# Optimization experiments

Hardware: AMD Instinct MI355X
Metric: run time of the kernel (lower is better)

## Reference

```python
import jax, jax.numpy as jnp
import numpy as np

N, E = 100000, 1600000
X_DIM, H_DIM, G_DIM = 128, 64, 64
Y_REP = H_DIM + G_DIM
N_OUT = 2


def setup_inputs() -> dict:
    key = jax.random.key(0)
    ks = jax.random.split(key, 16)
    features = jax.random.normal(ks[0], (N, X_DIM), dtype=jnp.float32)
    treatments = (jax.random.uniform(ks[1], (N,)) < 0.5).astype(jnp.float32)
    edge_index = jax.random.randint(ks[2], (2, E), 0, N, dtype=jnp.int64)
    s = 1.0 / np.sqrt(X_DIM)
    W_phi = jax.random.uniform(ks[3], (X_DIM, H_DIM), minval=-s, maxval=s, dtype=jnp.float32)
    b_phi = jax.random.uniform(ks[4], (H_DIM,), minval=-s, maxval=s, dtype=jnp.float32)
    sg = 1.0 / np.sqrt(H_DIM)
    W_gnn = jax.random.uniform(ks[5], (H_DIM, G_DIM), minval=-sg, maxval=sg, dtype=jnp.float32)
    b_gnn = jax.random.uniform(ks[6], (G_DIM,), minval=-sg, maxval=sg, dtype=jnp.float32)
    sy = 1.0 / np.sqrt(Y_REP)
    W00 = jax.random.uniform(ks[7], (N_OUT, Y_REP, Y_REP), minval=-sy, maxval=sy, dtype=jnp.float32)
    b00 = jax.random.uniform(ks[8], (N_OUT, Y_REP), minval=-sy, maxval=sy, dtype=jnp.float32)
    W10 = jax.random.uniform(ks[9], (N_OUT, Y_REP, Y_REP), minval=-sy, maxval=sy, dtype=jnp.float32)
    b10 = jax.random.uniform(ks[10], (N_OUT, Y_REP), minval=-sy, maxval=sy, dtype=jnp.float32)
    W01 = jax.random.uniform(ks[11], (Y_REP, 1), minval=-sy, maxval=sy, dtype=jnp.float32)
    b01 = jax.random.uniform(ks[12], (1,), minval=-sy, maxval=sy, dtype=jnp.float32)
    W11 = jax.random.uniform(ks[13], (Y_REP, 1), minval=-sy, maxval=sy, dtype=jnp.float32)
    b11 = jax.random.uniform(ks[14], (1,), minval=-sy, maxval=sy, dtype=jnp.float32)
    return dict(features=features, treatments=treatments, edge_index=edge_index,
                W_phi=W_phi, b_phi=b_phi, W_gnn=W_gnn, b_gnn=b_gnn,
                W00=W00, b00=b00, W10=W10, b10=b10,
                W01=W01, b01=b01, W11=W11, b11=b11)


def gcn_conv(x, edge_index, W, b, n_nodes):
    # PyG GCNConv defaults: add self-loops, symmetric deg^-1/2 normalization, bias.
    h = x @ W  # [N, G]
    loop = jnp.arange(n_nodes, dtype=edge_index.dtype)
    src = jnp.concatenate([edge_index[0], loop])
    dst = jnp.concatenate([edge_index[1], loop])
    deg = jax.ops.segment_sum(jnp.ones_like(dst, dtype=h.dtype), dst, num_segments=n_nodes)
    dinv = jnp.where(deg > 0, jax.lax.rsqrt(deg), 0.0)
    norm = dinv[src] * dinv[dst]  # [E+N]
    msg = h[src] * norm[:, None]  # gather + scale
    return jax.ops.segment_sum(msg, dst, num_segments=n_nodes) + b


def reference(features, treatments, edge_index, W_phi, b_phi, W_gnn, b_gnn,
              W00, b00, W10, b10, W01, b01, W11, b11):
    phi_x = jax.nn.relu(features @ W_phi + b_phi)  # [N, H]
    phi_x_t = treatments[:, None] * phi_x
    rep_gnn = gcn_conv(phi_x_t, edge_index, W_gnn, b_gnn, features.shape[0])  # [N, G]
    # dropout is a no-op in eval mode
    rep_post = jnp.concatenate([phi_x, rep_gnn], axis=1)  # [N, H+G]
    # faithful to the original: each iteration recomputes from rep_post (only last layer matters)
    for i in range(N_OUT):
        y00 = jax.nn.relu(rep_post @ W00[i] + b00[i])
        y10 = jax.nn.relu(rep_post @ W10[i] + b10[i])
    y0_pred = (y00 @ W01 + b01).reshape(-1)
    y1_pred = (y10 @ W11 + b11).reshape(-1)
    return y1_pred, y0_pred, phi_x
```

## Files before the change

### kernel.cpp

```cpp
#include <hip/hip_runtime.h>
#include <stdint.h>

typedef unsigned short u16;
typedef unsigned int u32;
typedef unsigned long long u64;
typedef long long ll;

#define XD 128
#define HD 64
#define GD 64
#define YREP 128
#define CAP 40

typedef __attribute__((ext_vector_type(8))) short bf16x8;
typedef __attribute__((ext_vector_type(4))) float f32x4;

#define SWT_LD  136
#define SF_LD   136
#define SO_LD   72

__device__ __forceinline__ float b2f(u16 x) { return __uint_as_float(((u32)x) << 16); }
__device__ __forceinline__ u16 f2b(float f) {
    u32 u = __float_as_uint(f);
    return (u16)((u + 0x7fffu + ((u >> 16) & 1u)) >> 16);
}
__device__ __forceinline__ float ldf(const void* p, size_t i, int bf) {
    return bf ? b2f(((const u16*)p)[i]) : ((const float*)p)[i];
}
__device__ __forceinline__ void stf(void* p, size_t i, float v, int bf) {
    if (bf) ((u16*)p)[i] = f2b(v);
    else ((float*)p)[i] = v;
}
__device__ __forceinline__ int ldi(const void* p, size_t i, int w) {
    return w ? (int)((const ll*)p)[i] : ((const int*)p)[i];
}
__device__ __forceinline__ bf16x8 ld_a8(const void* p, size_t off, int bf) {
    if (bf) return *(const bf16x8*)((const u16*)p + off);
    const float* fp = (const float*)p + off;
    bf16x8 a;
    #pragma unroll
    for (int i = 0; i < 8; ++i) a[i] = (short)f2b(fp[i]);
    return a;
}

__global__ void detect_kernel(const u32* __restrict__ treat_w,
                              const u32* __restrict__ eidx_w,
                              int* __restrict__ flags)
{
    int t = threadIdx.x;
    bool isbf = false, nzhi = false;
    for (int i = t; i < 256; i += 64) {
        isbf |= (treat_w[i] == 0x3F803F80u);
        nzhi |= (eidx_w[2 * i + 1] != 0u);
    }
    u64 mb = __ballot(isbf);
    u64 mn = __ballot(nzhi);
    if (t == 0) { flags[0] = mb ? 1 : 0; flags[1] = mn ? 0 : 1; }
}

__global__ __launch_bounds__(256) void wprep_kernel(
    const void* __restrict__ W00, const void* __restrict__ W10,
    const void* __restrict__ Wgnn, u32* __restrict__ WF,
    const int* __restrict__ flags)
{
    int bf = flags[0];
    int t = blockIdx.x * 256 + threadIdx.x;
    const void* src;
    size_t soff;
    int g, NKT, CDIM;
    u32* dst;
    if (t < 8192)       { src = W00;  soff = (size_t)YREP * YREP; g = t;         NKT = 4; CDIM = 128; dst = WF; }
    else if (t < 16384) { src = W10;  soff = (size_t)YREP * YREP; g = t - 8192;  NKT = 4; CDIM = 128; dst = WF + 8192; }
    else if (t < 18432) { src = Wgnn; soff = 0;                   g = t - 16384; NKT = 2; CDIM = 64;  dst = WF + 16384; }
    else return;
    int ep = g & 3, lane = (g >> 2) & 63, ctk = g >> 8;
    int kt = ctk % NKT, ct = ctk / NKT;
    int k = kt * 32 + (lane >> 4) * 8 + 2 * ep;
    int c = ct * 16 + (lane & 15);
    u32 lo = f2b(ldf(src, soff + (size_t)k * CDIM + c, bf));
    u32 hi = f2b(ldf(src, soff + (size_t)(k + 1) * CDIM + c, bf));
    dst[g] = lo | (hi << 16);
}

__global__ __launch_bounds__(512) void phi_mfma_kernel(
    const void* __restrict__ feat, const void* __restrict__ Wphi,
    const void* __restrict__ bphi, const void* __restrict__ treat,
    u32* __restrict__ mask, u32* __restrict__ cnt,
    void* __restrict__ dout, const int* __restrict__ flags, int N)
{
    __shared__ u16 sF[128 * SF_LD];
    __shared__ u16 sWT[64 * SWT_LD];
    u16* sOut = sF;

    int bf = flags[0];
    int tid = threadIdx.x;
    int lane = tid & 63;
    int w = tid >> 6;
    int row0 = blockIdx.x * 128;
    size_t pbase = 2 * (size_t)N;

    if (tid < 128) {
        int row = row0 + tid;
        bool t = (row < N) && (ldf(treat, row, bf) > 0.5f);
        u64 m = __ballot(t);
        int wbase = (row0 >> 5) + (tid >> 6) * 2;
        if (lane == 0)  mask[wbase]     = (u32)m;
        if (lane == 32) mask[wbase + 1] = (u32)(m >> 32);
        if (row < N) cnt[row] = 0;
    }

    if (bf) {
        for (int i = tid; i < 128 * 64; i += 512) {
            int r = i >> 6, k2 = i & 63;
            int row = row0 + r;
            u32 v = (row < N) ? ((const u32*)feat)[(size_t)row * 64 + k2] : 0u;
            ((u32*)sF)[r * (SF_LD / 2) + k2] = v;
        }
    } else {
        for (int i = tid; i < 128 * 64; i += 512) {
            int r = i >> 6, k2 = i & 63;
            int row = row0 + r;
            u32 v = 0;
            if (row < N) {
                const float* fp = (const float*)feat + (size_t)row * XD + 2 * k2;
                v = (u32)f2b(fp[0]) | ((u32)f2b(fp[1]) << 16);
            }
            ((u32*)sF)[r * (SF_LD / 2) + k2] = v;
        }
    }
    {
        int c = tid >> 3, kq = tid & 7;
        #pragma unroll
        for (int j = 0; j < 8; ++j) {
            int k = kq * 16 + 2 * j;
            u32 pk = (u32)f2b(ldf(Wphi, (size_t)k * HD + c, bf))
                   | ((u32)f2b(ldf(Wphi, (size_t)(k + 1) * HD + c, bf)) << 16);
            ((u32*)sWT)[(c * SWT_LD + k) >> 1] = pk;
        }
    }
    __syncthreads();

    f32x4 acc[4];
    #pragma unroll
    for (int ct = 0; ct < 4; ++ct) acc[ct] = (f32x4){0.f, 0.f, 0.f, 0.f};
    int r0 = w * 16;
    #pragma unroll
    for (int kt = 0; kt < 4; ++kt) {
        bf16x8 a = *(const bf16x8*)&sF[(r0 + (lane & 15)) * SF_LD + kt * 32 + (lane >> 4) * 8];
        #pragma unroll
        for (int ct = 0; ct < 4; ++ct) {
            bf16x8 b = *(const bf16x8*)&sWT[(ct * 16 + (lane & 15)) * SWT_LD + kt * 32 + (lane >> 4) * 8];
            acc[ct] = __builtin_amdgcn_mfma_f32_16x16x32_bf16(a, b, acc[ct], 0, 0, 0);
        }
    }
    __syncthreads();

    #pragma unroll
    for (int ct = 0; ct < 4; ++ct) {
        int c = ct * 16 + (lane & 15);
        float bl = ldf(bphi, c, bf);
        #pragma unroll
        for (int j = 0; j < 4; ++j) {
            float y = acc[ct][j] + bl;
            y = y > 0.f ? y : 0.f;
            sOut[(r0 + (lane >> 4) * 4 + j) * SO_LD + c] = f2b(y);
        }
    }
    __syncthreads();

    if (bf) {
        for (int i = tid; i < 128 * 32; i += 512) {
            int r = i >> 5, k2 = i & 31;
            int row = row0 + r;
            if (row < N)
                ((u32*)dout)[(pbase >> 1) + (size_t)row * 32 + k2] = ((u32*)sOut)[r * (SO_LD / 2) + k2];
        }
    } else {
        for (int i = tid; i < 128 * 64; i += 512) {
            int r = i >> 6, c = i & 63;
            int row = row0 + r;
            if (row < N)
                ((float*)dout)[pbase + (size_t)row * HD + c] = b2f(sOut[r * SO_LD + c]);
        }
    }
}

__global__ __launch_bounds__(256) void fill_slot_kernel(
    const void* __restrict__ eidx, u32* __restrict__ cnt,
    u32* __restrict__ slot, const u32* __restrict__ mask,
    const int* __restrict__ flags, int E)
{
    int i64 = flags[1];
    int tid = blockIdx.x * blockDim.x + threadIdx.x;
    int stride = gridDim.x * blockDim.x;

    int s[8], d[8];
    #pragma unroll
    for (int j = 0; j < 8; ++j) {
        int i = tid + j * stride;
        if (i < E) {
            s[j] = ldi(eidx, i, i64);
            d[j] = ldi(eidx, (size_t)E + i, i64);
        } else s[j] = -1;
    }
    u32 t[8];
    #pragma unroll
    for (int j = 0; j < 8; ++j)
        t[j] = (s[j] >= 0) ? ((mask[(u32)s[j] >> 5] >> ((u32)s[j] & 31)) & 1u) : 0u;
    u32 p[8];
    #pragma unroll
    for (int j = 0; j < 8; ++j)
        p[j] = (s[j] >= 0) ? atomicAdd(&cnt[d[j]], 0x10000u | t[j]) : 0u;
    #pragma unroll
    for (int j = 0; j < 8; ++j)
        if (s[j] >= 0 && t[j]) {
            u32 q = p[j] & 0xFFFFu;
            if (q < CAP) slot[(size_t)d[j] * CAP + q] = (u32)s[j];
        }
}

__global__ __launch_bounds__(256) void dinv_kernel(
    const u32* __restrict__ cnt, const void* __restrict__ treat,
    float* __restrict__ dinv, float* __restrict__ tw,
    const int* __restrict__ flags, int N)
{
    int bf = flags[0];
    int i = blockIdx.x * 256 + threadIdx.x;
    if (i >= N) return;
    float dv = rsqrtf((float)(cnt[i] >> 16) + 1.0f);
    dinv[i] = dv;
    tw[i] = dv * ldf(treat, i, bf);
}

__global__ __launch_bounds__(256) void gather_slot_kernel(
    const void* __restrict__ dout, const u32* __restrict__ cnt,
    const u32* __restrict__ slot, const float* __restrict__ dinv,
    const float* __restrict__ tw, u16* __restrict__ agg,
    const int* __restrict__ flags, int N)
{
    int bf = flags[0];
    int lane = threadIdx.x & 63;
    int n = (blockIdx.x * 256 + threadIdx.x) >> 6;
    if (n >= N) return;
    size_t pbase = 2 * (size_t)N;
    float acc = ldf(dout, pbase + (size_t)n * HD + lane, bf) * tw[n];
    u32 kept = cnt[n] & 0xFFFFu; if (kept > CAP) kept = CAP;
    const u32* row = &slot[(size_t)n * CAP];
    for (u32 j0 = 0; j0 < kept; j0 += 8) {
        u32 s[8];
        #pragma unroll
        for (int j = 0; j < 8; ++j)
            s[j] = (j0 + j < kept) ? row[j0 + j] : 0xFFFFFFFFu;
        float wg[8];
        #pragma unroll
        for (int j = 0; j < 8; ++j)
            wg[j] = (s[j] != 0xFFFFFFFFu) ? dinv[s[j]] : 0.f;
        #pragma unroll
        for (int j = 0; j < 8; ++j)
            if (s[j] != 0xFFFFFFFFu)
                acc += ldf(dout, pbase + (size_t)s[j] * HD + lane, bf) * wg[j];
    }
    agg[(size_t)n * HD + lane] = f2b(acc * dinv[n]);
}

__device__ __forceinline__ void head_mfma_phase2(
    const void* __restrict__ dout, const u16* __restrict__ sGnn,
    const u32* __restrict__ WFh,
    const void* __restrict__ bvec,
    const void* __restrict__ Wlin, float blin,
    size_t yoff, int row0, int N, int lane, int w, int bf,
    bool aval, int arow, size_t pbase, void* dst)
{
    f32x4 acc[8];
    #pragma unroll
    for (int ct = 0; ct < 8; ++ct) acc[ct] = (f32x4){0.f, 0.f, 0.f, 0.f};

    #pragma unroll
    for (int kt = 0; kt < 4; ++kt) {
        bf16x8 a;
        if (kt < 2) {
            #pragma unroll
            for (int i = 0; i < 8; ++i) a[i] = 0;
            if (aval) a = ld_a8(dout, pbase + (size_t)arow * HD + kt * 32 + (lane >> 4) * 8, bf);
        } else {
            a = *(const bf16x8*)&sGnn[((w * 2 + (kt - 2)) * 64 + lane) * 8];
        }
        #pragma unroll
        for (int ct = 0; ct < 8; ++ct) {
            bf16x8 b = *(const bf16x8*)&WFh[((ct * 4 + kt) * 64 + lane) * 4];
            acc[ct] = __builtin_amdgcn_mfma_f32_16x16x32_bf16(a, b, acc[ct], 0, 0, 0);
        }
    }
    float p0 = 0.f, p1 = 0.f, p2 = 0.f, p3 = 0.f;
    #pragma unroll
    for (int ct = 0; ct < 8; ++ct) {
        int c = ct * 16 + (lane & 15);
        float bl = ldf(bvec, (size_t)YREP + c, bf);
        float wl = ldf(Wlin, c, bf);
        float y0 = acc[ct][0] + bl; y0 = y0 > 0.f ? y0 : 0.f; p0 += y0 * wl;
        float y1 = acc[ct][1] + bl; y1 = y1 > 0.f ? y1 : 0.f; p1 += y1 * wl;
        float y2 = acc[ct][2] + bl; y2 = y2 > 0.f ? y2 : 0.f; p2 += y2 * wl;
        float y3 = acc[ct][3] + bl; y3 = y3 > 0.f ? y3 : 0.f; p3 += y3 * wl;
    }
    float p[4] = {p0, p1, p2, p3};
    #pragma unroll
    for (int j = 0; j < 4; ++j) {
        #pragma unroll
        for (int m = 8; m >= 1; m >>= 1)
            p[j] += __shfl_xor(p[j], m, 64);
        if ((lane & 15) == 0) {
            int row = row0 + w * 16 + (lane >> 4) * 4 + j;
            if (row < N) stf(dst, yoff + row, p[j] + blin, bf);
        }
    }
}

__global__ __launch_bounds__(512) void head_kernel(
    void* __restrict__ dout, const u16* __restrict__ agg,
    const u32* __restrict__ WF, const void* __restrict__ bgnn,
    const void* __restrict__ b00, const void* __restrict__ b10,
    const void* __restrict__ W01, const void* __restrict__ b01,
    const void* __restrict__ W11, const void* __restrict__ b11,
    const int* __restrict__ flags, int N)
{
    __shared__ u16 sGnn[8192];

    int bf = flags[0];
    int tid = threadIdx.x;
    int lane = tid & 63;
    int w = tid >> 6;
    int l15 = lane & 15;
    int hi = lane >> 4;
    int row0 = blockIdx.x * 128;
    size_t pbase = 2 * (size_t)N;
    int arow = row0 + w * 16 + l15;
    bool aval = arow < N;

    {
        const u32* WgF = WF + 16384;
        f32x4 g[4];
        #pragma unroll
        for (int ct = 0; ct < 4; ++ct) g[ct] = (f32x4){0.f, 0.f, 0.f, 0.f};
        #pragma unroll
        for (int kt = 0; kt < 2; ++kt) {
            bf16x8 a;
            #pragma unroll
            for (int i = 0; i < 8; ++i) a[i] = 0;
            if (aval) a = *(const bf16x8*)&agg[(size_t)arow * HD + kt * 32 + hi * 8];
            #pragma unroll
            for (int ct = 0; ct < 4; ++ct) {
                bf16x8 b = *(const bf16x8*)&WgF[((ct * 2 + kt) * 64 + lane) * 4];
                g[ct] = __builtin_amdgcn_mfma_f32_16x16x32_bf16(a, b, g[ct], 0, 0, 0);
            }
        }
        #pragma unroll
        for (int ct = 0; ct < 4; ++ct) {
            int c = ct * 16 + l15;
            float bg = ldf(bgnn, c, bf);
            int kt2 = c >> 5, hh = (c >> 3) & 3, e = c & 7;
            #pragma unroll
            for (int j = 0; j < 4; ++j) {
                int r = hi * 4 + j;
                sGnn[(((w * 2 + kt2) * 64) + hh * 16 + r) * 8 + e] = f2b(g[ct][j] + bg);
            }
        }
    }
    __syncthreads();

    head_mfma_phase2(dout, sGnn, WF, b00, W01, ldf(b01, 0, bf),
                     (size_t)N, row0, N, lane, w, bf, aval, arow, pbase, dout);
    head_mfma_phase2(dout, sGnn, WF + 8192, b10, W11, ldf(b11, 0, bf),
                     (size_t)0, row0, N, lane, w, bf, aval, arow, pbase, dout);
}

extern "C" void kernel_launch(void* const* d_in, const int* in_sizes, int n_in,
                              void* d_out, int out_size, void* d_ws, size_t ws_size,
                              hipStream_t stream)
{
    const void* feat  = d_in[0];
    const void* treat = d_in[1];
    const void* eidx  = d_in[2];
    const void* Wphi  = d_in[3];
    const void* bphi  = d_in[4];
    const void* Wgnn  = d_in[5];
    const void* bgnn  = d_in[6];
    const void* W00   = d_in[7];
    const void* b00   = d_in[8];
    const void* W10   = d_in[9];
    const void* b10   = d_in[10];
    const void* W01   = d_in[11];
    const void* b01   = d_in[12];
    const void* W11   = d_in[13];
    const void* b11   = d_in[14];

    const int N = in_sizes[1];
    const int E = in_sizes[2] / 2;
    const int NBLK = (N + 127) / 128;

    char* w = (char*)d_ws;
    size_t off = 0;
    auto alloc = [&](size_t bytes) { void* p = w + off; off += (bytes + 255) & ~(size_t)255; return p; };

    int*   flags = (int*)alloc(256);
    u32*   cnt   = (u32*)alloc((size_t)N * 4);
    float* dinv  = (float*)alloc((size_t)N * 4);
    float* tw    = (float*)alloc((size_t)N * 4);
    u32*   mask  = (u32*)alloc((size_t)NBLK * 4 * 4);
    u32*   WF    = (u32*)alloc((size_t)18432 * 4);
    u32*   slot  = (u32*)alloc((size_t)N * CAP * 4);
    u16*   agg   = (u16*)alloc((size_t)N * HD * 2);

    detect_kernel<<<1, 64, 0, stream>>>((const u32*)treat, (const u32*)eidx, flags);

    wprep_kernel<<<72, 256, 0, stream>>>(W00, W10, Wgnn, WF, flags);

    phi_mfma_kernel<<<NBLK, 512, 0, stream>>>(
        feat, Wphi, bphi, treat, mask, cnt, d_out, flags, N);

    fill_slot_kernel<<<1024, 256, 0, stream>>>(eidx, cnt, slot, mask, flags, E);

    dinv_kernel<<<(N + 255) / 256, 256, 0, stream>>>(cnt, treat, dinv, tw, flags, N);

    gather_slot_kernel<<<(N + 3) / 4, 256, 0, stream>>>(
        d_out, cnt, slot, dinv, tw, agg, flags, N);

    head_kernel<<<NBLK, 512, 0, stream>>>(
        d_out, agg, WF, bgnn, b00, b10, W01, b01, W11, b11, flags, N);
}
```

Measured before the change: 240.2 us.

## Fuse prep kernels, co-schedule edge fill with phi GEMM, compute dinv inline

Merges format detection, weight repacking, mask and count init into one prep kernel. The edge slot-fill pass now runs in extra leading blocks of the phi MFMA kernel, so the latency-bound atomics overlap with the GEMM blocks. The dinv/tw kernel is dropped, and gather recomputes rsqrt from the counts and the treatment bit from the mask. This removes three launches and their serialization, at the cost of a random cnt load per neighbor in gather and a heavier block mix in the fused kernel.

```diff
diff --git a/kernel.cpp b/kernel.cpp
--- a/kernel.cpp
+++ b/kernel.cpp
@@ -11,6 +11,7 @@
 #define GD 64
 #define YREP 128
 #define CAP 40
+#define FBLK 512
 
 typedef __attribute__((ext_vector_type(8))) short bf16x8;
 typedef __attribute__((ext_vector_type(4))) float f32x4;
@@ -43,50 +44,67 @@
     return a;
 }
 
-__global__ void detect_kernel(const u32* __restrict__ treat_w,
-                              const u32* __restrict__ eidx_w,
-                              int* __restrict__ flags)
-{
-    int t = threadIdx.x;
-    bool isbf = false, nzhi = false;
-    for (int i = t; i < 256; i += 64) {
-        isbf |= (treat_w[i] == 0x3F803F80u);
-        nzhi |= (eidx_w[2 * i + 1] != 0u);
-    }
-    u64 mb = __ballot(isbf);
-    u64 mn = __ballot(nzhi);
-    if (t == 0) { flags[0] = mb ? 1 : 0; flags[1] = mn ? 0 : 1; }
-}
-
-__global__ __launch_bounds__(256) void wprep_kernel(
+__global__ __launch_bounds__(256) void prep_kernel(
+    const u32* __restrict__ treat_w, const u32* __restrict__ eidx_w,
+    const void* __restrict__ treat,
     const void* __restrict__ W00, const void* __restrict__ W10,
-    const void* __restrict__ Wgnn, u32* __restrict__ WF,
-    const int* __restrict__ flags)
-{
-    int bf = flags[0];
-    int t = blockIdx.x * 256 + threadIdx.x;
-    const void* src;
-    size_t soff;
-    int g, NKT, CDIM;
-    u32* dst;
-    if (t < 8192)       { src = W00;  soff = (size_t)YREP * YREP; g = t;         NKT = 4; CDIM = 128; dst = WF; }
-    else if (t < 16384) { src = W10;  soff = (size_t)YREP * YREP; g = t - 8192;  NKT = 4; CDIM = 128; dst = WF + 8192; }
-    else if (t < 18432) { src = Wgnn; soff = 0;                   g = t - 16384; NKT = 2; CDIM = 64;  dst = WF + 16384; }
-    else return;
-    int ep = g & 3, lane = (g >> 2) & 63, ctk = g >> 8;
-    int kt = ctk % NKT, ct = ctk / NKT;
-    int k = kt * 32 + (lane >> 4) * 8 + 2 * ep;
-    int c = ct * 16 + (lane & 15);
-    u32 lo = f2b(ldf(src, soff + (size_t)k * CDIM + c, bf));
-    u32 hi = f2b(ldf(src, soff + (size_t)(k + 1) * CDIM + c, bf));
-    dst[g] = lo | (hi << 16);
-}
-
-__global__ __launch_bounds__(512) void phi_mfma_kernel(
+    const void* __restrict__ Wgnn,
+    int* __restrict__ flags, u32* __restrict__ mask, u32* __restrict__ cnt,
+    u32* __restrict__ WF, int N)
+{
+    __shared__ int sdet[2];
+    int tid = threadIdx.x;
+    if (tid < 64) {
+        bool isbf = false, nzhi = false;
+        for (int i = tid; i < 256; i += 64) {
+            isbf |= (treat_w[i] == 0x3F803F80u);
+            nzhi |= (eidx_w[2 * i + 1] != 0u);
+        }
+        u64 mb = __ballot(isbf);
+        u64 mn = __ballot(nzhi);
+        if (tid == 0) {
+            sdet[0] = mb ? 1 : 0;
+            sdet[1] = mn ? 0 : 1;
+            if (blockIdx.x == 0) { flags[0] = sdet[0]; flags[1] = sdet[1]; }
+        }
+    }
+    __syncthreads();
+    int bf = sdet[0];
+
+    int row = blockIdx.x * 256 + tid;
+    bool t = (row < N) && (ldf(treat, row, bf) > 0.5f);
+    u64 m = __ballot(t);
+    int lane = tid & 63;
+    int wbase = blockIdx.x * 8 + (tid >> 6) * 2;
+    if (lane == 0)  mask[wbase]     = (u32)m;
+    if (lane == 32) mask[wbase + 1] = (u32)(m >> 32);
+    if (row < N) cnt[row] = 0;
+
+    int g = blockIdx.x * 256 + tid;
+    if (g < 18432) {
+        const void* src;
+        size_t soff;
+        int gg, NKT, CDIM;
+        u32* dst;
+        if (g < 8192)       { src = W00;  soff = (size_t)YREP * YREP; gg = g;         NKT = 4; CDIM = 128; dst = WF; }
+        else if (g < 16384) { src = W10;  soff = (size_t)YREP * YREP; gg = g - 8192;  NKT = 4; CDIM = 128; dst = WF + 8192; }
+        else                { src = Wgnn; soff = 0;                   gg = g - 16384; NKT = 2; CDIM = 64;  dst = WF + 16384; }
+        int ep = gg & 3, ln = (gg >> 2) & 63, ctk = gg >> 8;
+        int kt = ctk % NKT, ct = ctk / NKT;
+        int k = kt * 32 + (ln >> 4) * 8 + 2 * ep;
+        int c = ct * 16 + (ln & 15);
+        u32 lo = f2b(ldf(src, soff + (size_t)k * CDIM + c, bf));
+        u32 hi = f2b(ldf(src, soff + (size_t)(k + 1) * CDIM + c, bf));
+        dst[gg] = lo | (hi << 16);
+    }
+}
+
+__global__ __launch_bounds__(512) void phifill_kernel(
     const void* __restrict__ feat, const void* __restrict__ Wphi,
-    const void* __restrict__ bphi, const void* __restrict__ treat,
-    u32* __restrict__ mask, u32* __restrict__ cnt,
-    void* __restrict__ dout, const int* __restrict__ flags, int N)
+    const void* __restrict__ bphi, const void* __restrict__ eidx,
+    u32* __restrict__ cnt, u32* __restrict__ slot,
+    const u32* __restrict__ mask, void* __restrict__ dout,
+    const int* __restrict__ flags, int N, int E)
 {
     __shared__ u16 sF[128 * SF_LD];
     __shared__ u16 sWT[64 * SWT_LD];
@@ -94,20 +112,41 @@
 
     int bf = flags[0];
     int tid = threadIdx.x;
+
+    if (blockIdx.x < FBLK) {
+        int i64 = flags[1];
+        int ftid = blockIdx.x * 512 + tid;
+        int stride = FBLK * 512;
+        int s[8], d[8];
+        #pragma unroll
+        for (int j = 0; j < 8; ++j) {
+            int i = ftid + j * stride;
+            if (i < E) {
+                s[j] = ldi(eidx, i, i64);
+                d[j] = ldi(eidx, (size_t)E + i, i64);
+            } else s[j] = -1;
+        }
+        u32 t[8];
+        #pragma unroll
+        for (int j = 0; j < 8; ++j)
+            t[j] = (s[j] >= 0) ? ((mask[(u32)s[j] >> 5] >> ((u32)s[j] & 31)) & 1u) : 0u;
+        u32 p[8];
+        #pragma unroll
+        for (int j = 0; j < 8; ++j)
+            p[j] = (s[j] >= 0) ? atomicAdd(&cnt[d[j]], 0x10000u | t[j]) : 0u;
+        #pragma unroll
+        for (int j = 0; j < 8; ++j)
+            if (s[j] >= 0 && t[j]) {
+                u32 q = p[j] & 0xFFFFu;
+                if (q < CAP) slot[(size_t)d[j] * CAP + q] = (u32)s[j];
+            }
+        return;
+    }
+
     int lane = tid & 63;
     int w = tid >> 6;
-    int row0 = blockIdx.x * 128;
+    int row0 = (blockIdx.x - FBLK) * 128;
     size_t pbase = 2 * (size_t)N;
-
-    if (tid < 128) {
-        int row = row0 + tid;
-        bool t = (row < N) && (ldf(treat, row, bf) > 0.5f);
-        u64 m = __ballot(t);
-        int wbase = (row0 >> 5) + (tid >> 6) * 2;
-        if (lane == 0)  mask[wbase]     = (u32)m;
-        if (lane == 32) mask[wbase + 1] = (u32)(m >> 32);
-        if (row < N) cnt[row] = 0;
-    }
 
     if (bf) {
         for (int i = tid; i < 128 * 64; i += 512) {
@@ -185,66 +224,21 @@
     }
 }
 
-__global__ __launch_bounds__(256) void fill_slot_kernel(
-    const void* __restrict__ eidx, u32* __restrict__ cnt,
-    u32* __restrict__ slot, const u32* __restrict__ mask,
-    const int* __restrict__ flags, int E)
-{
-    int i64 = flags[1];
-    int tid = blockIdx.x * blockDim.x + threadIdx.x;
-    int stride = gridDim.x * blockDim.x;
-
-    int s[8], d[8];
-    #pragma unroll
-    for (int j = 0; j < 8; ++j) {
-        int i = tid + j * stride;
-        if (i < E) {
-            s[j] = ldi(eidx, i, i64);
-            d[j] = ldi(eidx, (size_t)E + i, i64);
-        } else s[j] = -1;
-    }
-    u32 t[8];
-    #pragma unroll
-    for (int j = 0; j < 8; ++j)
-        t[j] = (s[j] >= 0) ? ((mask[(u32)s[j] >> 5] >> ((u32)s[j] & 31)) & 1u) : 0u;
-    u32 p[8];
-    #pragma unroll
-    for (int j = 0; j < 8; ++j)
-        p[j] = (s[j] >= 0) ? atomicAdd(&cnt[d[j]], 0x10000u | t[j]) : 0u;
-    #pragma unroll
-    for (int j = 0; j < 8; ++j)
-        if (s[j] >= 0 && t[j]) {
-            u32 q = p[j] & 0xFFFFu;
-            if (q < CAP) slot[(size_t)d[j] * CAP + q] = (u32)s[j];
-        }
-}
-
-__global__ __launch_bounds__(256) void dinv_kernel(
-    const u32* __restrict__ cnt, const void* __restrict__ treat,
-    float* __restrict__ dinv, float* __restrict__ tw,
-    const int* __restrict__ flags, int N)
-{
-    int bf = flags[0];
-    int i = blockIdx.x * 256 + threadIdx.x;
-    if (i >= N) return;
-    float dv = rsqrtf((float)(cnt[i] >> 16) + 1.0f);
-    dinv[i] = dv;
-    tw[i] = dv * ldf(treat, i, bf);
-}
-
 __global__ __launch_bounds__(256) void gather_slot_kernel(
     const void* __restrict__ dout, const u32* __restrict__ cnt,
-    const u32* __restrict__ slot, const float* __restrict__ dinv,
-    const float* __restrict__ tw, u16* __restrict__ agg,
-    const int* __restrict__ flags, int N)
+    const u32* __restrict__ slot, const u32* __restrict__ mask,
+    u16* __restrict__ agg, const int* __restrict__ flags, int N)
 {
     int bf = flags[0];
     int lane = threadIdx.x & 63;
     int n = (blockIdx.x * 256 + threadIdx.x) >> 6;
     if (n >= N) return;
     size_t pbase = 2 * (size_t)N;
-    float acc = ldf(dout, pbase + (size_t)n * HD + lane, bf) * tw[n];
-    u32 kept = cnt[n] & 0xFFFFu; if (kept > CAP) kept = CAP;
+    u32 cn = cnt[n];
+    float dvn = rsqrtf((float)(cn >> 16) + 1.0f);
+    u32 tb = (mask[(u32)n >> 5] >> ((u32)n & 31)) & 1u;
+    float acc = ldf(dout, pbase + (size_t)n * HD + lane, bf) * (dvn * (float)tb);
+    u32 kept = cn & 0xFFFFu; if (kept > CAP) kept = CAP;
     const u32* row = &slot[(size_t)n * CAP];
     for (u32 j0 = 0; j0 < kept; j0 += 8) {
         u32 s[8];
@@ -254,13 +248,14 @@
         float wg[8];
         #pragma unroll
         for (int j = 0; j < 8; ++j)
-            wg[j] = (s[j] != 0xFFFFFFFFu) ? dinv[s[j]] : 0.f;
+            wg[j] = (s[j] != 0xFFFFFFFFu)
+                  ? rsqrtf((float)(cnt[s[j]] >> 16) + 1.0f) : 0.f;
         #pragma unroll
         for (int j = 0; j < 8; ++j)
             if (s[j] != 0xFFFFFFFFu)
                 acc += ldf(dout, pbase + (size_t)s[j] * HD + lane, bf) * wg[j];
     }
-    agg[(size_t)n * HD + lane] = f2b(acc * dinv[n]);
+    agg[(size_t)n * HD + lane] = f2b(acc * dvn);
 }
 
 __device__ __forceinline__ void head_mfma_phase2(
@@ -396,6 +391,7 @@
     const int N = in_sizes[1];
     const int E = in_sizes[2] / 2;
     const int NBLK = (N + 127) / 128;
+    const int PBLK = (N + 255) / 256;
 
     char* w = (char*)d_ws;
     size_t off = 0;
@@ -403,26 +399,20 @@
 
     int*   flags = (int*)alloc(256);
     u32*   cnt   = (u32*)alloc((size_t)N * 4);
-    float* dinv  = (float*)alloc((size_t)N * 4);
-    float* tw    = (float*)alloc((size_t)N * 4);
-    u32*   mask  = (u32*)alloc((size_t)NBLK * 4 * 4);
+    u32*   mask  = (u32*)alloc((size_t)PBLK * 8 * 4);
     u32*   WF    = (u32*)alloc((size_t)18432 * 4);
     u32*   slot  = (u32*)alloc((size_t)N * CAP * 4);
     u16*   agg   = (u16*)alloc((size_t)N * HD * 2);
 
-    detect_kernel<<<1, 64, 0, stream>>>((const u32*)treat, (const u32*)eidx, flags);
-
-    wprep_kernel<<<72, 256, 0, stream>>>(W00, W10, Wgnn, WF, flags);
-
-    phi_mfma_kernel<<<NBLK, 512, 0, stream>>>(
-        feat, Wphi, bphi, treat, mask, cnt, d_out, flags, N);
-
-    fill_slot_kernel<<<1024, 256, 0, stream>>>(eidx, cnt, slot, mask, flags, E);
-
-    dinv_kernel<<<(N + 255) / 256, 256, 0, stream>>>(cnt, treat, dinv, tw, flags, N);
+    prep_kernel<<<PBLK, 256, 0, stream>>>(
+        (const u32*)treat, (const u32*)eidx, treat, W00, W10, Wgnn,
+        flags, mask, cnt, WF, N);
+
+    phifill_kernel<<<FBLK + NBLK, 512, 0, stream>>>(
+        feat, Wphi, bphi, eidx, cnt, slot, mask, d_out, flags, N, E);
 
     gather_slot_kernel<<<(N + 3) / 4, 256, 0, stream>>>(
-        d_out, cnt, slot, dinv, tw, agg, flags, N);
+        d_out, cnt, slot, mask, agg, flags, N);
 
     head_kernel<<<NBLK, 512, 0, stream>>>(
         d_out, agg, WF, bgnn, b00, b10, W01, b01, W11, b11, flags, N);
```

Measured after the change: 246.2 us. +2.5%, slower.
